# Kernel tuning notes

Hardware: AMD Instinct MI355X
Metric: run time of the kernel (lower is better)

Reference implementation:

```python
import jax, jax.numpy as jnp
import numpy as np

B, C, H, W = 16, 256, 32, 32
N_E, E_DIM = 8192, 256
BETA = 0.25
ENT_RATIO = 0.1
TEMP = 0.01


def _normalize(x, eps=1e-6):
    # torch F.normalize: x / clamp_min(||x||, eps)
    n = jnp.linalg.norm(x, axis=-1, keepdims=True)
    return x / jnp.maximum(n, eps)


def setup_inputs() -> dict:
    key = jax.random.key(0)
    k1, k2, k3 = jax.random.split(key, 3)
    z = jax.random.normal(k1, (B, C, H, W), dtype=jnp.float32)
    # nn.Embedding init: normal(0, e_dim**-0.5)
    emb_weight = jax.random.normal(k2, (N_E, E_DIM), dtype=jnp.float32) * (E_DIM ** -0.5)
    # nn.Linear(e_dim, e_dim)
    proj_w = jax.random.normal(k3, (E_DIM, E_DIM), dtype=jnp.float32) * (E_DIM ** -0.5)
    proj_b = jnp.zeros((E_DIM,), dtype=jnp.float32)
    return {"z": z, "emb_weight": emb_weight, "proj_w": proj_w, "proj_b": proj_b}


def reference(z, emb_weight, proj_w, proj_b):
    sg = jax.lax.stop_gradient
    # SimVQ: project the (frozen) codebook through a linear layer
    weight = emb_weight @ proj_w.T + proj_b            # [K, d]
    b, c, h, w = z.shape
    z_bhwc = jnp.transpose(z, (0, 2, 3, 1))            # [B,H,W,C]
    z_flat = z_bhwc.reshape(b, h * w, c)               # [B,L,C]

    # l2_norm=True branch
    zn = _normalize(z_flat)                             # [B,L,d]
    wn = _normalize(weight)                             # [K,d]

    z2 = jnp.sum(zn * zn, axis=-1, keepdims=True)       # [B,L,1]
    w2 = jnp.sum(wn * wn, axis=-1)[None, None, :]       # [1,1,K]
    dot = jnp.einsum('bld,kd->blk', zn, wn)             # [B,L,K]
    dists = z2 + w2 - 2.0 * dot                         # [B,L,K]

    indices = jnp.argmin(dists, axis=-1)                # [B,L]
    q = wn[indices].reshape(b, h, w, c)                 # gather normalized codebook

    # training losses (l2_norm=True -> compare normalized)
    z_cmp = _normalize(z_bhwc)
    q_cmp = _normalize(q)
    codebook_loss = jnp.mean((q_cmp - sg(z_cmp)) ** 2)
    commit_loss = BETA * jnp.mean((sg(q_cmp) - z_cmp) ** 2)

    # entropy loss on affinity = -dists
    a = (-dists).reshape(-1, dists.shape[-1]) / TEMP    # [B*L, K]
    probs = jax.nn.softmax(a, axis=-1)
    log_probs = jax.nn.log_softmax(a + 1e-5, axis=-1)
    avg_probs = jnp.mean(probs, axis=0)
    avg_entropy = -jnp.sum(avg_probs * jnp.log(avg_probs + 1e-5))
    sample_entropy = -jnp.mean(jnp.sum(probs * log_probs, axis=-1))
    entropy_loss = ENT_RATIO * (sample_entropy - avg_entropy)

    # straight-through estimator, back to channel-first
    z_q = z_bhwc + sg(q - z_bhwc)
    z_q = jnp.transpose(z_q, (0, 3, 1, 2))              # [B,C,H,W]
    flat_indices = indices.reshape(-1)
    return (z_q, codebook_loss, commit_loss, entropy_loss, flat_indices)
```

## Files before the change

### kernel.cpp

```cpp
#include <hip/hip_runtime.h>
#include <math.h>

#define NROWS 16384
#define NCODES 8192
#define DIMS 256
#define NCS 4
#define CEXP 288.5390082f

#define OFF_WN   0u
#define OFF_W2   2097152u
#define OFF_ZN   2105344u
#define OFF_WNH  6299648u
#define OFF_WNL  7348224u
#define OFF_ZNH  8396800u
#define OFF_ZNL  10493952u
#define OFF_PL1  12591104u
#define OFF_PL2  12656640u
#define OFF_PS   12722176u
#define OFF_PI1  12787712u
#define OFF_PI2  12853248u
#define OFF_RM   12918784u
#define OFF_RS   12935168u
#define OFF_RIDX 12951552u
#define OFF_AVGP 12967936u
#define OFF_SCAL 12976128u

typedef __attribute__((ext_vector_type(8))) short bf16x8;
typedef __attribute__((ext_vector_type(4))) float f32x4;
typedef unsigned short u16;

__device__ __forceinline__ u16 f2bf(float f) {
  unsigned u = __float_as_uint(f);
  u += 0x7fffu + ((u >> 16) & 1u);
  return (u16)(u >> 16);
}
__device__ __forceinline__ float bf2f(u16 s) { return __uint_as_float(((unsigned)s) << 16); }

__device__ __forceinline__ void gl_lds16(const u16* g, u16* l) {
  __builtin_amdgcn_global_load_lds(
      (const __attribute__((address_space(1))) unsigned*)g,
      (__attribute__((address_space(3))) unsigned*)l, 16, 0, 0);
}

#define PHASE_BARRIER_CNT()  asm volatile("s_waitcnt vmcnt(4) lgkmcnt(0)\n\ts_barrier" ::: "memory")
#define PHASE_BARRIER_ALL()  asm volatile("s_waitcnt vmcnt(0) lgkmcnt(0)\n\ts_barrier" ::: "memory")
#define DRAIN_VM()           asm volatile("s_waitcnt vmcnt(0)" ::: "memory")

__device__ __forceinline__ void ins2(float x, int idx, float& b1, int& i1, float& b2, int& i2) {
  if (x > b1 || (x == b1 && idx < i1)) { b2 = b1; i2 = i1; b1 = x; i1 = idx; }
  else if (x > b2 || (x == b2 && idx < i2)) { b2 = x; i2 = idx; }
}

__global__ __launch_bounds__(256) void k0_init(float* ws) {
  int i = blockIdx.x * 256 + threadIdx.x;
  if (i < NCODES) ws[OFF_AVGP + i] = 0.f;
  if (i < 16) ws[OFF_SCAL + i] = 0.f;
}

__global__ __launch_bounds__(256) void k1_codebook(const float* __restrict__ emb,
    const float* __restrict__ pw, const float* __restrict__ pb,
    float* __restrict__ wn, float* __restrict__ w2,
    u16* __restrict__ wnh, u16* __restrict__ wnl) {
  __shared__ float e[256];
  __shared__ float red[256];
  int k = blockIdx.x, t = threadIdx.x;
  e[t] = emb[(size_t)k * 256 + t];
  __syncthreads();
  const float4* prow = reinterpret_cast<const float4*>(pw + (size_t)t * 256);
  float acc = pb[t];
  #pragma unroll 8
  for (int q = 0; q < 64; ++q) {
    float4 p4 = prow[q];
    acc += e[q*4+0]*p4.x + e[q*4+1]*p4.y + e[q*4+2]*p4.z + e[q*4+3]*p4.w;
  }
  red[t] = acc * acc;
  __syncthreads();
  for (int s = 128; s; s >>= 1) { if (t < s) red[t] += red[t+s]; __syncthreads(); }
  float inv = 1.f / fmaxf(sqrtf(red[0]), 1e-6f);
  float v = acc * inv;
  size_t o = (size_t)k*256 + t;
  wn[o] = v;
  u16 hb = f2bf(v); float hf = bf2f(hb);
  wnh[o] = hb; wnl[o] = f2bf(v - hf);
  __syncthreads();
  red[t] = v * v;
  __syncthreads();
  for (int s = 128; s; s >>= 1) { if (t < s) red[t] += red[t+s]; __syncthreads(); }
  if (t == 0) w2[k] = red[0];
}

__global__ __launch_bounds__(256) void k2_zn(const float* __restrict__ z,
    float* __restrict__ zn, u16* __restrict__ znh, u16* __restrict__ znl) {
  __shared__ float tile[256][33];
  __shared__ float inv[32];
  int bh = blockIdx.x, t = threadIdx.x;
  const float* zb = z + (size_t)(bh >> 5) * (256*1024) + (size_t)(bh & 31) * 32;
  for (int j = 0; j < 32; ++j) {
    int i = t + j*256; int c = i >> 5, w = i & 31;
    tile[c][w] = zb[(size_t)c*1024 + w];
  }
  __syncthreads();
  if (t < 32) {
    float s = 0.f;
    for (int c = 0; c < 256; ++c) { float v = tile[c][t]; s += v*v; }
    inv[t] = 1.f / fmaxf(sqrtf(s), 1e-6f);
  }
  __syncthreads();
  size_t base = (size_t)bh * 32 * 256;
  for (int w = 0; w < 32; ++w) {
    float v = tile[t][w] * inv[w];
    size_t o = base + (size_t)w*256 + t;
    zn[o] = v;
    u16 hb = f2bf(v); float hf = bf2f(hb);
    znh[o] = hb; znl[o] = f2bf(v - hf);
  }
}

__global__ __attribute__((amdgpu_flat_work_group_size(512,512)))
__attribute__((amdgpu_waves_per_eu(2,2))) void k3_pass1(
    const u16* __restrict__ znh, const u16* __restrict__ znl,
    const u16* __restrict__ wnh, const u16* __restrict__ wnl,
    float* __restrict__ pL1, float* __restrict__ pL2, float* __restrict__ pS,
    int* __restrict__ pI1, int* __restrict__ pI2) {
  __shared__ u16 Cbuf[6][2][128*32];
  int t = threadIdx.x;
  int rb = blockIdx.x >> 2, cs = blockIdx.x & 3;
  int r0 = rb * 256;
  int w = t >> 6, l = t & 63;
  int g = l >> 4, lr = l & 15;
  int slotA = ((lr >> 1) & 3);

  bf16x8 bh[2][8], bl[2][8];
  #pragma unroll
  for (int jr = 0; jr < 2; ++jr) {
    size_t rbase = (size_t)(r0 + w*32 + jr*16 + lr) * 256;
    #pragma unroll
    for (int dc = 0; dc < 8; ++dc) {
      bh[jr][dc] = *(const bf16x8*)&znh[rbase + dc*32 + g*8];
      bl[jr][dc] = *(const bf16x8*)&znl[rbase + dc*32 + g*8];
    }
  }
  #pragma unroll
  for (int jr = 0; jr < 2; ++jr)
    #pragma unroll
    for (int dc = 0; dc < 8; ++dc)
      asm volatile("" : "+v"(bh[jr][dc]), "+v"(bl[jr][dc]));

  const size_t csbase = (size_t)cs * 2048 * 256;
  auto stage = [&](int s, int b) {
    int dc2 = s & 7;
    int krow = (s >> 3) * 128;
    int c = w*16 + (l >> 2);
    int qs = (l & 3) ^ ((l >> 3) & 3);
    size_t go = csbase + (size_t)(krow + c)*256 + dc2*32 + qs*8;
    gl_lds16(&wnh[go], &Cbuf[b][0][w*512]);
    gl_lds16(&wnl[go], &Cbuf[b][1][w*512]);
  };
  DRAIN_VM();
  stage(0, 0);
  stage(1, 1);
  stage(2, 2);
  stage(3, 3);

  float b1[2] = {-3.0e38f, -3.0e38f}, b2[2] = {-3.0e38f, -3.0e38f}, Sv[2] = {0.f, 0.f};
  int i1[2] = {0, 0}, i2[2] = {0, 0};

  for (int kt = 0; kt < 16; ++kt) {
    f32x4 acc[8][2];
    #pragma unroll
    for (int i = 0; i < 8; ++i) { acc[i][0] = (f32x4){0.f,0.f,0.f,0.f}; acc[i][1] = (f32x4){0.f,0.f,0.f,0.f}; }
    #pragma unroll
    for (int dcp = 0; dcp < 4; ++dcp) {
      int s0 = kt*8 + dcp*2;
      if (s0 < 126) PHASE_BARRIER_CNT(); else PHASE_BARRIER_ALL();
      if (s0 + 4 < 128) { int b4 = (s0+4) % 6; stage(s0 + 4, b4); }
      if (s0 + 5 < 128) { int b5 = (s0+5) % 6; stage(s0 + 5, b5); }
      #pragma unroll
      for (int h = 0; h < 2; ++h) {
        int dc = dcp*2 + h;
        int bR = (s0 + h) % 6;
        #pragma unroll
        for (int i = 0; i < 8; ++i) {
          int co = (i*16 + lr)*32 + (g ^ slotA)*8;
          bf16x8 ah = *(const bf16x8*)&Cbuf[bR][0][co];
          bf16x8 al = *(const bf16x8*)&Cbuf[bR][1][co];
          acc[i][0] = __builtin_amdgcn_mfma_f32_16x16x32_bf16(ah, bh[0][dc], acc[i][0], 0, 0, 0);
          acc[i][1] = __builtin_amdgcn_mfma_f32_16x16x32_bf16(ah, bh[1][dc], acc[i][1], 0, 0, 0);
          acc[i][0] = __builtin_amdgcn_mfma_f32_16x16x32_bf16(ah, bl[0][dc], acc[i][0], 0, 0, 0);
          acc[i][1] = __builtin_amdgcn_mfma_f32_16x16x32_bf16(ah, bl[1][dc], acc[i][1], 0, 0, 0);
          acc[i][0] = __builtin_amdgcn_mfma_f32_16x16x32_bf16(al, bh[0][dc], acc[i][0], 0, 0, 0);
          acc[i][1] = __builtin_amdgcn_mfma_f32_16x16x32_bf16(al, bh[1][dc], acc[i][1], 0, 0, 0);
        }
      }
    }
    int kb32 = kt * 32;
    #pragma unroll
    for (int jr = 0; jr < 2; ++jr) {
      float ob1 = b1[jr];
      #pragma unroll
      for (int n = 0; n < 32; ++n) {
        float x = acc[n>>2][jr][n&3];
        bool c1 = x > b1[jr];
        bool c2 = x > b2[jr];
        float hi = fmaxf(x, b1[jr]);
        float lo = fminf(x, b1[jr]);
        b2[jr] = fmaxf(lo, fminf(hi, b2[jr]));
        i2[jr] = c1 ? i1[jr] : (c2 ? (kb32 + n) : i2[jr]);
        b1[jr] = hi;
        i1[jr] = c1 ? (kb32 + n) : i1[jr];
      }
      float negCm = -CEXP * b1[jr];
      float ts0 = 0.f, ts1 = 0.f;
      #pragma unroll
      for (int n = 0; n < 32; n += 2) {
        ts0 += exp2f(fmaf(CEXP, acc[n>>2][jr][n&3],     negCm));
        ts1 += exp2f(fmaf(CEXP, acc[(n+1)>>2][jr][(n+1)&3], negCm));
      }
      Sv[jr] = Sv[jr] * exp2f(CEXP * (ob1 - b1[jr])) + (ts0 + ts1);
    }
  }
  float my[2], y2[2]; int gi1[2], gi2[2];
  #pragma unroll
  for (int jr = 0; jr < 2; ++jr) {
    int e1 = i1[jr], e2 = i2[jr];
    int base = cs*2048 + g*4;
    gi1[jr] = base + (e1>>5)*128 + ((e1>>2)&7)*16 + (e1&3);
    gi2[jr] = base + (e2>>5)*128 + ((e2>>2)&7)*16 + (e2&3);
    my[jr] = CEXP * b1[jr];
    y2[jr] = CEXP * b2[jr];
    #pragma unroll
    for (int mask = 16; mask <= 32; mask <<= 1) {
      float om  = __shfl_xor(my[jr], mask, 64);
      float oy2 = __shfl_xor(y2[jr], mask, 64);
      float oS  = __shfl_xor(Sv[jr], mask, 64);
      int   o1  = __shfl_xor(gi1[jr], mask, 64);
      int   o2  = __shfl_xor(gi2[jr], mask, 64);
      float pm = my[jr];
      ins2(om,  o1, my[jr], gi1[jr], y2[jr], gi2[jr]);
      ins2(oy2, o2, my[jr], gi1[jr], y2[jr], gi2[jr]);
      Sv[jr] = Sv[jr] * exp2f(pm - my[jr]) + oS * exp2f(om - my[jr]);
    }
  }
  if (g == 0) {
    #pragma unroll
    for (int jr = 0; jr < 2; ++jr) {
      int r = r0 + w*32 + jr*16 + lr;
      size_t o = (size_t)cs * NROWS + r;
      pL1[o] = my[jr]; pL2[o] = y2[jr]; pS[o] = Sv[jr];
      pI1[o] = gi1[jr]; pI2[o] = gi2[jr];
    }
  }
}

__global__ __launch_bounds__(256) void k3b_refine(
    const float* __restrict__ zn, const float* __restrict__ wn, const float* __restrict__ w2,
    const float* __restrict__ pL1, const float* __restrict__ pL2, const float* __restrict__ pS,
    const int* __restrict__ pI1, const int* __restrict__ pI2,
    float* __restrict__ rm, float* __restrict__ rs, int* __restrict__ ridx) {
  int t = threadIdx.x;
  int r = blockIdx.x * 4 + (t >> 6);
  int l = t & 63;
  float b1 = pL1[r], b2 = pL2[r], S = pS[r];
  int i1 = pI1[r], i2 = pI2[r];
  #pragma unroll
  for (int c = 1; c < NCS; ++c) {
    size_t o = (size_t)c * NROWS + r;
    float ob1 = pL1[o], ob2 = pL2[o], oS = pS[o];
    int oi1 = pI1[o], oi2 = pI2[o];
    float pb1 = b1;
    ins2(ob1, oi1, b1, i1, b2, i2);
    ins2(ob2, oi2, b1, i1, b2, i2);
    S = S * exp2f(pb1 - b1) + oS * exp2f(ob1 - b1);
  }
  int cand = (l < 32) ? i1 : i2;
  int lo = l & 31;
  const float* zr = zn + (size_t)r * 256;
  const float* wc = wn + (size_t)cand * 256;
  float d = 0.f;
  #pragma unroll
  for (int q = 0; q < 8; ++q) d += zr[lo + q*32] * wc[lo + q*32];
  #pragma unroll
  for (int mask = 1; mask <= 16; mask <<= 1) d += __shfl_xor(d, mask, 64);
  float dOther = __shfl_xor(d, 32, 64);
  if (l == 0) {
    float s1 = w2[i1] - 2.f*d;
    float s2 = w2[i2] - 2.f*dOther;
    int win = i1;
    if (s2 < s1 || (s2 == s1 && i2 < i1)) win = i2;
    rm[r] = b1; rs[r] = S; ridx[r] = win;
  }
}

__global__ __attribute__((amdgpu_flat_work_group_size(512,512)))
__attribute__((amdgpu_waves_per_eu(2,2))) void k4_pass2(
    const u16* __restrict__ znh, const u16* __restrict__ znl,
    const u16* __restrict__ wnh, const u16* __restrict__ wnl,
    const float* __restrict__ rm, const float* __restrict__ rs,
    float* __restrict__ avgp, float* __restrict__ scal) {
  __shared__ u16 Cbuf[6][2][128*32];
  __shared__ float avgSlice[2048];
  __shared__ float red[512];
  int t = threadIdx.x;
  int rb = blockIdx.x >> 2, cs = blockIdx.x & 3;
  int r0 = rb * 256;
  int w = t >> 6, l = t & 63;
  int g = l >> 4, lr = l & 15;
  int slotA = ((lr >> 1) & 3);

  for (int i = t; i < 2048; i += 512) avgSlice[i] = 0.f;

  bf16x8 bh[2][8], bl[2][8];
  #pragma unroll
  for (int jr = 0; jr < 2; ++jr) {
    size_t rbase = (size_t)(r0 + w*32 + jr*16 + lr) * 256;
    #pragma unroll
    for (int dc = 0; dc < 8; ++dc) {
      bh[jr][dc] = *(const bf16x8*)&znh[rbase + dc*32 + g*8];
      bl[jr][dc] = *(const bf16x8*)&znl[rbase + dc*32 + g*8];
    }
  }
  #pragma unroll
  for (int jr = 0; jr < 2; ++jr)
    #pragma unroll
    for (int dc = 0; dc < 8; ++dc)
      asm volatile("" : "+v"(bh[jr][dc]), "+v"(bl[jr][dc]));

  float m_[2], invS[2], l2s[2];
  #pragma unroll
  for (int jr = 0; jr < 2; ++jr) {
    int r = r0 + w*32 + jr*16 + lr;
    float mm = rm[r], ss = rs[r];
    m_[jr] = mm; invS[jr] = 1.f / ss; l2s[jr] = log2f(ss);
  }

  const size_t csbase = (size_t)cs * 2048 * 256;
  auto stage = [&](int s, int b) {
    int dc2 = s & 7;
    int krow = (s >> 3) * 128;
    int c = w*16 + (l >> 2);
    int qs = (l & 3) ^ ((l >> 3) & 3);
    size_t go = csbase + (size_t)(krow + c)*256 + dc2*32 + qs*8;
    gl_lds16(&wnh[go], &Cbuf[b][0][w*512]);
    gl_lds16(&wnl[go], &Cbuf[b][1][w*512]);
  };
  DRAIN_VM();
  stage(0, 0);
  stage(1, 1);
  stage(2, 2);
  stage(3, 3);
  float ent = 0.f;

  for (int kt = 0; kt < 16; ++kt) {
    f32x4 acc[8][2];
    #pragma unroll
    for (int i = 0; i < 8; ++i) { acc[i][0] = (f32x4){0.f,0.f,0.f,0.f}; acc[i][1] = (f32x4){0.f,0.f,0.f,0.f}; }
    #pragma unroll
    for (int dcp = 0; dcp < 4; ++dcp) {
      int s0 = kt*8 + dcp*2;
      if (s0 < 126) PHASE_BARRIER_CNT(); else PHASE_BARRIER_ALL();
      if (s0 + 4 < 128) { int b4 = (s0+4) % 6; stage(s0 + 4, b4); }
      if (s0 + 5 < 128) { int b5 = (s0+5) % 6; stage(s0 + 5, b5); }
      #pragma unroll
      for (int h = 0; h < 2; ++h) {
        int dc = dcp*2 + h;
        int bR = (s0 + h) % 6;
        #pragma unroll
        for (int i = 0; i < 8; ++i) {
          int co = (i*16 + lr)*32 + (g ^ slotA)*8;
          bf16x8 ah = *(const bf16x8*)&Cbuf[bR][0][co];
          bf16x8 al = *(const bf16x8*)&Cbuf[bR][1][co];
          acc[i][0] = __builtin_amdgcn_mfma_f32_16x16x32_bf16(ah, bh[0][dc], acc[i][0], 0, 0, 0);
          acc[i][1] = __builtin_amdgcn_mfma_f32_16x16x32_bf16(ah, bh[1][dc], acc[i][1], 0, 0, 0);
          acc[i][0] = __builtin_amdgcn_mfma_f32_16x16x32_bf16(ah, bl[0][dc], acc[i][0], 0, 0, 0);
          acc[i][1] = __builtin_amdgcn_mfma_f32_16x16x32_bf16(ah, bl[1][dc], acc[i][1], 0, 0, 0);
          acc[i][0] = __builtin_amdgcn_mfma_f32_16x16x32_bf16(al, bh[0][dc], acc[i][0], 0, 0, 0);
          acc[i][1] = __builtin_amdgcn_mfma_f32_16x16x32_bf16(al, bh[1][dc], acc[i][1], 0, 0, 0);
        }
      }
    }
    #pragma unroll
    for (int half = 0; half < 2; ++half) {
      float ca[16];
      #pragma unroll
      for (int n = 0; n < 16; ++n) ca[n] = 0.f;
      #pragma unroll
      for (int jr = 0; jr < 2; ++jr) {
        float is = invS[jr], l2 = l2s[jr];
        #pragma unroll
        for (int ii = 0; ii < 4; ++ii) {
          int i = half*4 + ii;
          #pragma unroll
          for (int v = 0; v < 4; ++v) {
            float tt = fmaf(CEXP, acc[i][jr][v], -m_[jr]);
            float p = exp2f(tt) * is;
            ent -= p * (tt - l2);
            ca[ii*4+v] += p;
          }
        }
      }
      #pragma unroll
      for (int n = 0; n < 16; ++n) {
        float sv = ca[n];
        sv += __shfl_xor(sv, 1, 64);
        sv += __shfl_xor(sv, 2, 64);
        sv += __shfl_xor(sv, 4, 64);
        sv += __shfl_xor(sv, 8, 64);
        if (lr == 0)
          atomicAdd(&avgSlice[kt*128 + (half*4 + (n>>2))*16 + g*4 + (n&3)], sv);
      }
    }
  }
  __syncthreads();
  for (int i = t; i < 2048; i += 512)
    atomicAdd(&avgp[cs*2048 + i], avgSlice[i] * (1.f/16384.f));
  red[t] = ent;
  __syncthreads();
  for (int s2 = 256; s2; s2 >>= 1) { if (t < s2) red[t] += red[t + s2]; __syncthreads(); }
  if (t == 0) atomicAdd(&scal[1], red[0] * 0.6931471806f);
}

__global__ __launch_bounds__(256) void k5_gather(const float* __restrict__ zn,
    const float* __restrict__ wn, const int* __restrict__ row_idx,
    float* __restrict__ out_zq, float* __restrict__ scal) {
  __shared__ float tile[256][33];
  __shared__ float red4[4];
  __shared__ float red[256];
  int bh = blockIdx.x, t = threadIdx.x;
  int b = bh >> 5, h = bh & 31;
  float cb = 0.f;
  for (int w = 0; w < 32; ++w) {
    int r = bh*32 + w;
    int idx = row_idx[r];
    float q = wn[(size_t)idx*256 + t];
    float s = q*q;
    #pragma unroll
    for (int mask = 32; mask; mask >>= 1) s += __shfl_xor(s, mask, 64);
    if ((t & 63) == 0) red4[t >> 6] = s;
    __syncthreads();
    float tot = red4[0] + red4[1] + red4[2] + red4[3];
    float inv = 1.f / fmaxf(sqrtf(tot), 1e-6f);
    float zv = zn[(size_t)r*256 + t];
    float d = q*inv - zv;
    cb += d*d;
    tile[t][w] = q;
    __syncthreads();
  }
  red[t] = cb;
  __syncthreads();
  for (int s2 = 128; s2; s2 >>= 1) { if (t < s2) red[t] += red[t+s2]; __syncthreads(); }
  if (t == 0) atomicAdd(&scal[0], red[0]);
  float* ob = out_zq + (size_t)b*256*1024 + (size_t)h*32;
  for (int j = 0; j < 32; ++j) {
    int i = t + j*256; int c = i >> 5, ww = i & 31;
    ob[(size_t)c*1024 + ww] = tile[c][ww];
  }
}

__global__ __launch_bounds__(256) void k6_final(const float* __restrict__ avg_probs,
    const float* __restrict__ scal, const int* __restrict__ row_idx,
    float* __restrict__ out) {
  int t = threadIdx.x;
  if (blockIdx.x < 64) {
    int r = blockIdx.x*256 + t;
    out[4194307 + r] = (float)row_idx[r];
    return;
  }
  __shared__ float red[256];
  float s = 0.f;
  for (int j = 0; j < 32; ++j) {
    float v = avg_probs[t + j*256];
    s -= v * logf(v + 1e-5f);
  }
  red[t] = s;
  __syncthreads();
  for (int q = 128; q; q >>= 1) { if (t < q) red[t] += red[t+q]; __syncthreads(); }
  if (t == 0) {
    float avg_entropy = red[0];
    float sample_entropy = scal[1] * (1.f/16384.f);
    float cb = scal[0] * (1.f/4194304.f);
    out[4194304] = cb;
    out[4194305] = 0.25f * cb;
    out[4194306] = 0.1f * (sample_entropy - avg_entropy);
  }
}

extern "C" void kernel_launch(void* const* d_in, const int* in_sizes, int n_in,
                              void* d_out, int out_size, void* d_ws, size_t ws_size,
                              hipStream_t stream) {
  const float* z   = (const float*)d_in[0];
  const float* emb = (const float*)d_in[1];
  const float* pw  = (const float*)d_in[2];
  const float* pb  = (const float*)d_in[3];
  float* ws  = (float*)d_ws;
  float* out = (float*)d_out;
  float* wn   = ws + OFF_WN;
  float* w2   = ws + OFF_W2;
  float* zn   = ws + OFF_ZN;
  u16*   wnh  = (u16*)(ws + OFF_WNH);
  u16*   wnl  = (u16*)(ws + OFF_WNL);
  u16*   znh  = (u16*)(ws + OFF_ZNH);
  u16*   znl  = (u16*)(ws + OFF_ZNL);
  float* pL1  = ws + OFF_PL1;
  float* pL2  = ws + OFF_PL2;
  float* pS   = ws + OFF_PS;
  int*   pI1  = (int*)(ws + OFF_PI1);
  int*   pI2  = (int*)(ws + OFF_PI2);
  float* rm   = ws + OFF_RM;
  float* rs   = ws + OFF_RS;
  int*   ridx = (int*)(ws + OFF_RIDX);
  float* avgp = ws + OFF_AVGP;
  float* scal = ws + OFF_SCAL;

  k0_init<<<32, 256, 0, stream>>>(ws);
  k1_codebook<<<NCODES, 256, 0, stream>>>(emb, pw, pb, wn, w2, wnh, wnl);
  k2_zn<<<512, 256, 0, stream>>>(z, zn, znh, znl);
  k3_pass1<<<256, 512, 0, stream>>>(znh, znl, wnh, wnl, pL1, pL2, pS, pI1, pI2);
  k3b_refine<<<NROWS/4, 256, 0, stream>>>(zn, wn, w2, pL1, pL2, pS, pI1, pI2, rm, rs, ridx);
  k4_pass2<<<256, 512, 0, stream>>>(znh, znl, wnh, wnl, rm, rs, avgp, scal);
  k5_gather<<<512, 256, 0, stream>>>(zn, wn, ridx, out, scal);
  k6_final<<<65, 256, 0, stream>>>(avgp, scal, ridx, out);
}
```

Measured before the change: 782.1 us.

## Halve rows per block in both GEMM passes and double the grid size

```diff
diff --git a/kernel.cpp b/kernel.cpp
--- a/kernel.cpp
+++ b/kernel.cpp
@@ -125,26 +125,20 @@
   __shared__ u16 Cbuf[6][2][128*32];
   int t = threadIdx.x;
   int rb = blockIdx.x >> 2, cs = blockIdx.x & 3;
-  int r0 = rb * 256;
+  int r0 = rb * 128;
   int w = t >> 6, l = t & 63;
   int g = l >> 4, lr = l & 15;
   int slotA = ((lr >> 1) & 3);
 
-  bf16x8 bh[2][8], bl[2][8];
-  #pragma unroll
-  for (int jr = 0; jr < 2; ++jr) {
-    size_t rbase = (size_t)(r0 + w*32 + jr*16 + lr) * 256;
+  bf16x8 bh[8], bl[8];
+  {
+    size_t rbase = (size_t)(r0 + w*16 + lr) * 256;
     #pragma unroll
     for (int dc = 0; dc < 8; ++dc) {
-      bh[jr][dc] = *(const bf16x8*)&znh[rbase + dc*32 + g*8];
-      bl[jr][dc] = *(const bf16x8*)&znl[rbase + dc*32 + g*8];
-    }
-  }
-  #pragma unroll
-  for (int jr = 0; jr < 2; ++jr)
-    #pragma unroll
-    for (int dc = 0; dc < 8; ++dc)
-      asm volatile("" : "+v"(bh[jr][dc]), "+v"(bl[jr][dc]));
+      bh[dc] = *(const bf16x8*)&znh[rbase + dc*32 + g*8];
+      bl[dc] = *(const bf16x8*)&znl[rbase + dc*32 + g*8];
+    }
+  }
 
   const size_t csbase = (size_t)cs * 2048 * 256;
   auto stage = [&](int s, int b) {
@@ -162,13 +156,13 @@
   stage(2, 2);
   stage(3, 3);
 
-  float b1[2] = {-3.0e38f, -3.0e38f}, b2[2] = {-3.0e38f, -3.0e38f}, Sv[2] = {0.f, 0.f};
-  int i1[2] = {0, 0}, i2[2] = {0, 0};
+  float b1 = -3.0e38f, b2 = -3.0e38f, Sv = 0.f;
+  int i1 = 0, i2 = 0;
 
   for (int kt = 0; kt < 16; ++kt) {
-    f32x4 acc[8][2];
-    #pragma unroll
-    for (int i = 0; i < 8; ++i) { acc[i][0] = (f32x4){0.f,0.f,0.f,0.f}; acc[i][1] = (f32x4){0.f,0.f,0.f,0.f}; }
+    f32x4 acc[8];
+    #pragma unroll
+    for (int i = 0; i < 8; ++i) acc[i] = (f32x4){0.f,0.f,0.f,0.f};
     #pragma unroll
     for (int dcp = 0; dcp < 4; ++dcp) {
       int s0 = kt*8 + dcp*2;
@@ -184,71 +178,62 @@
           int co = (i*16 + lr)*32 + (g ^ slotA)*8;
           bf16x8 ah = *(const bf16x8*)&Cbuf[bR][0][co];
           bf16x8 al = *(const bf16x8*)&Cbuf[bR][1][co];
-          acc[i][0] = __builtin_amdgcn_mfma_f32_16x16x32_bf16(ah, bh[0][dc], acc[i][0], 0, 0, 0);
-          acc[i][1] = __builtin_amdgcn_mfma_f32_16x16x32_bf16(ah, bh[1][dc], acc[i][1], 0, 0, 0);
-          acc[i][0] = __builtin_amdgcn_mfma_f32_16x16x32_bf16(ah, bl[0][dc], acc[i][0], 0, 0, 0);
-          acc[i][1] = __builtin_amdgcn_mfma_f32_16x16x32_bf16(ah, bl[1][dc], acc[i][1], 0, 0, 0);
-          acc[i][0] = __builtin_amdgcn_mfma_f32_16x16x32_bf16(al, bh[0][dc], acc[i][0], 0, 0, 0);
-          acc[i][1] = __builtin_amdgcn_mfma_f32_16x16x32_bf16(al, bh[1][dc], acc[i][1], 0, 0, 0);
+          acc[i] = __builtin_amdgcn_mfma_f32_16x16x32_bf16(ah, bh[dc], acc[i], 0, 0, 0);
+          acc[i] = __builtin_amdgcn_mfma_f32_16x16x32_bf16(ah, bl[dc], acc[i], 0, 0, 0);
+          acc[i] = __builtin_amdgcn_mfma_f32_16x16x32_bf16(al, bh[dc], acc[i], 0, 0, 0);
         }
       }
     }
     int kb32 = kt * 32;
-    #pragma unroll
-    for (int jr = 0; jr < 2; ++jr) {
-      float ob1 = b1[jr];
+    {
+      float ob1 = b1;
       #pragma unroll
       for (int n = 0; n < 32; ++n) {
-        float x = acc[n>>2][jr][n&3];
-        bool c1 = x > b1[jr];
-        bool c2 = x > b2[jr];
-        float hi = fmaxf(x, b1[jr]);
-        float lo = fminf(x, b1[jr]);
-        b2[jr] = fmaxf(lo, fminf(hi, b2[jr]));
-        i2[jr] = c1 ? i1[jr] : (c2 ? (kb32 + n) : i2[jr]);
-        b1[jr] = hi;
-        i1[jr] = c1 ? (kb32 + n) : i1[jr];
-      }
-      float negCm = -CEXP * b1[jr];
+        float x = acc[n>>2][n&3];
+        bool c1 = x > b1;
+        bool c2 = x > b2;
+        float hi = fmaxf(x, b1);
+        float lo = fminf(x, b1);
+        b2 = fmaxf(lo, fminf(hi, b2));
+        i2 = c1 ? i1 : (c2 ? (kb32 + n) : i2);
+        b1 = hi;
+        i1 = c1 ? (kb32 + n) : i1;
+      }
+      float negCm = -CEXP * b1;
       float ts0 = 0.f, ts1 = 0.f;
       #pragma unroll
       for (int n = 0; n < 32; n += 2) {
-        ts0 += exp2f(fmaf(CEXP, acc[n>>2][jr][n&3],     negCm));
-        ts1 += exp2f(fmaf(CEXP, acc[(n+1)>>2][jr][(n+1)&3], negCm));
-      }
-      Sv[jr] = Sv[jr] * exp2f(CEXP * (ob1 - b1[jr])) + (ts0 + ts1);
-    }
-  }
-  float my[2], y2[2]; int gi1[2], gi2[2];
-  #pragma unroll
-  for (int jr = 0; jr < 2; ++jr) {
-    int e1 = i1[jr], e2 = i2[jr];
+        ts0 += exp2f(fmaf(CEXP, acc[n>>2][n&3],         negCm));
+        ts1 += exp2f(fmaf(CEXP, acc[(n+1)>>2][(n+1)&3], negCm));
+      }
+      Sv = Sv * exp2f(CEXP * (ob1 - b1)) + (ts0 + ts1);
+    }
+  }
+  float my, y2; int gi1, gi2;
+  {
     int base = cs*2048 + g*4;
-    gi1[jr] = base + (e1>>5)*128 + ((e1>>2)&7)*16 + (e1&3);
-    gi2[jr] = base + (e2>>5)*128 + ((e2>>2)&7)*16 + (e2&3);
-    my[jr] = CEXP * b1[jr];
-    y2[jr] = CEXP * b2[jr];
+    gi1 = base + (i1>>5)*128 + ((i1>>2)&7)*16 + (i1&3);
+    gi2 = base + (i2>>5)*128 + ((i2>>2)&7)*16 + (i2&3);
+    my = CEXP * b1;
+    y2 = CEXP * b2;
     #pragma unroll
     for (int mask = 16; mask <= 32; mask <<= 1) {
-      float om  = __shfl_xor(my[jr], mask, 64);
-      float oy2 = __shfl_xor(y2[jr], mask, 64);
-      float oS  = __shfl_xor(Sv[jr], mask, 64);
-      int   o1  = __shfl_xor(gi1[jr], mask, 64);
-      int   o2  = __shfl_xor(gi2[jr], mask, 64);
-      float pm = my[jr];
-      ins2(om,  o1, my[jr], gi1[jr], y2[jr], gi2[jr]);
-      ins2(oy2, o2, my[jr], gi1[jr], y2[jr], gi2[jr]);
-      Sv[jr] = Sv[jr] * exp2f(pm - my[jr]) + oS * exp2f(om - my[jr]);
+      float om  = __shfl_xor(my, mask, 64);
+      float oy2 = __shfl_xor(y2, mask, 64);
+      float oS  = __shfl_xor(Sv, mask, 64);
+      int   o1  = __shfl_xor(gi1, mask, 64);
+      int   o2  = __shfl_xor(gi2, mask, 64);
+      float pm = my;
+      ins2(om,  o1, my, gi1, y2, gi2);
+      ins2(oy2, o2, my, gi1, y2, gi2);
+      Sv = Sv * exp2f(pm - my) + oS * exp2f(om - my);
     }
   }
   if (g == 0) {
-    #pragma unroll
-    for (int jr = 0; jr < 2; ++jr) {
-      int r = r0 + w*32 + jr*16 + lr;
-      size_t o = (size_t)cs * NROWS + r;
-      pL1[o] = my[jr]; pL2[o] = y2[jr]; pS[o] = Sv[jr];
-      pI1[o] = gi1[jr]; pI2[o] = gi2[jr];
-    }
+    int r = r0 + w*16 + lr;
+    size_t o = (size_t)cs * NROWS + r;
+    pL1[o] = my; pL2[o] = y2; pS[o] = Sv;
+    pI1[o] = gi1; pI2[o] = gi2;
   }
 }
 
@@ -302,35 +287,27 @@
   __shared__ float red[512];
   int t = threadIdx.x;
   int rb = blockIdx.x >> 2, cs = blockIdx.x & 3;
-  int r0 = rb * 256;
+  int r0 = rb * 128;
   int w = t >> 6, l = t & 63;
   int g = l >> 4, lr = l & 15;
   int slotA = ((lr >> 1) & 3);
 
   for (int i = t; i < 2048; i += 512) avgSlice[i] = 0.f;
 
-  bf16x8 bh[2][8], bl[2][8];
-  #pragma unroll
-  for (int jr = 0; jr < 2; ++jr) {
-    size_t rbase = (size_t)(r0 + w*32 + jr*16 + lr) * 256;
+  bf16x8 bh[8], bl[8];
+  {
+    size_t rbase = (size_t)(r0 + w*16 + lr) * 256;
     #pragma unroll
     for (int dc = 0; dc < 8; ++dc) {
-      bh[jr][dc] = *(const bf16x8*)&znh[rbase + dc*32 + g*8];
-      bl[jr][dc] = *(const bf16x8*)&znl[rbase + dc*32 + g*8];
-    }
-  }
-  #pragma unroll
-  for (int jr = 0; jr < 2; ++jr)
-    #pragma unroll
-    for (int dc = 0; dc < 8; ++dc)
-      asm volatile("" : "+v"(bh[jr][dc]), "+v"(bl[jr][dc]));
-
-  float m_[2], invS[2], l2s[2];
-  #pragma unroll
-  for (int jr = 0; jr < 2; ++jr) {
-    int r = r0 + w*32 + jr*16 + lr;
+      bh[dc] = *(const bf16x8*)&znh[rbase + dc*32 + g*8];
+      bl[dc] = *(const bf16x8*)&znl[rbase + dc*32 + g*8];
+    }
+  }
+  float m_, invS, l2s;
+  {
+    int r = r0 + w*16 + lr;
     float mm = rm[r], ss = rs[r];
-    m_[jr] = mm; invS[jr] = 1.f / ss; l2s[jr] = log2f(ss);
+    m_ = mm; invS = 1.f / ss; l2s = log2f(ss);
   }
 
   const size_t csbase = (size_t)cs * 2048 * 256;
@@ -351,9 +328,9 @@
   float ent = 0.f;
 
   for (int kt = 0; kt < 16; ++kt) {
-    f32x4 acc[8][2];
-    #pragma unroll
-    for (int i = 0; i < 8; ++i) { acc[i][0] = (f32x4){0.f,0.f,0.f,0.f}; acc[i][1] = (f32x4){0.f,0.f,0.f,0.f}; }
+    f32x4 acc[8];
+    #pragma unroll
+    for (int i = 0; i < 8; ++i) acc[i] = (f32x4){0.f,0.f,0.f,0.f};
     #pragma unroll
     for (int dcp = 0; dcp < 4; ++dcp) {
       int s0 = kt*8 + dcp*2;
@@ -369,33 +346,27 @@
           int co = (i*16 + lr)*32 + (g ^ slotA)*8;
           bf16x8 ah = *(const bf16x8*)&Cbuf[bR][0][co];
           bf16x8 al = *(const bf16x8*)&Cbuf[bR][1][co];
-          acc[i][0] = __builtin_amdgcn_mfma_f32_16x16x32_bf16(ah, bh[0][dc], acc[i][0], 0, 0, 0);
-          acc[i][1] = __builtin_amdgcn_mfma_f32_16x16x32_bf16(ah, bh[1][dc], acc[i][1], 0, 0, 0);
-          acc[i][0] = __builtin_amdgcn_mfma_f32_16x16x32_bf16(ah, bl[0][dc], acc[i][0], 0, 0, 0);
-          acc[i][1] = __builtin_amdgcn_mfma_f32_16x16x32_bf16(ah, bl[1][dc], acc[i][1], 0, 0, 0);
-          acc[i][0] = __builtin_amdgcn_mfma_f32_16x16x32_bf16(al, bh[0][dc], acc[i][0], 0, 0, 0);
-          acc[i][1] = __builtin_amdgcn_mfma_f32_16x16x32_bf16(al, bh[1][dc], acc[i][1], 0, 0, 0);
+          acc[i] = __builtin_amdgcn_mfma_f32_16x16x32_bf16(ah, bh[dc], acc[i], 0, 0, 0);
+          acc[i] = __builtin_amdgcn_mfma_f32_16x16x32_bf16(ah, bl[dc], acc[i], 0, 0, 0);
+          acc[i] = __builtin_amdgcn_mfma_f32_16x16x32_bf16(al, bh[dc], acc[i], 0, 0, 0);
         }
       }
     }
+    int kb = cs*2048 + kt*128;
     #pragma unroll
     for (int half = 0; half < 2; ++half) {
       float ca[16];
       #pragma unroll
       for (int n = 0; n < 16; ++n) ca[n] = 0.f;
       #pragma unroll
-      for (int jr = 0; jr < 2; ++jr) {
-        float is = invS[jr], l2 = l2s[jr];
+      for (int ii = 0; ii < 4; ++ii) {
+        int i = half*4 + ii;
         #pragma unroll
-        for (int ii = 0; ii < 4; ++ii) {
-          int i = half*4 + ii;
-          #pragma unroll
-          for (int v = 0; v < 4; ++v) {
-            float tt = fmaf(CEXP, acc[i][jr][v], -m_[jr]);
-            float p = exp2f(tt) * is;
-            ent -= p * (tt - l2);
-            ca[ii*4+v] += p;
-          }
+        for (int v = 0; v < 4; ++v) {
+          float tt = fmaf(CEXP, acc[i][v], -m_);
+          float p = exp2f(tt) * invS;
+          ent -= p * (tt - l2s);
+          ca[ii*4+v] += p;
         }
       }
       #pragma unroll
@@ -514,9 +485,9 @@
   k0_init<<<32, 256, 0, stream>>>(ws);
   k1_codebook<<<NCODES, 256, 0, stream>>>(emb, pw, pb, wn, w2, wnh, wnl);
   k2_zn<<<512, 256, 0, stream>>>(z, zn, znh, znl);
-  k3_pass1<<<256, 512, 0, stream>>>(znh, znl, wnh, wnl, pL1, pL2, pS, pI1, pI2);
+  k3_pass1<<<512, 512, 0, stream>>>(znh, znl, wnh, wnl, pL1, pL2, pS, pI1, pI2);
   k3b_refine<<<NROWS/4, 256, 0, stream>>>(zn, wn, w2, pL1, pL2, pS, pI1, pI2, rm, rs, ridx);
-  k4_pass2<<<256, 512, 0, stream>>>(znh, znl, wnh, wnl, rm, rs, avgp, scal);
+  k4_pass2<<<512, 512, 0, stream>>>(znh, znl, wnh, wnl, rm, rs, avgp, scal);
   k5_gather<<<512, 256, 0, stream>>>(zn, wn, ridx, out, scal);
   k6_final<<<65, 256, 0, stream>>>(avgp, scal, ridx, out);
 }
```

After: 889.6 us. +13.7%, slower.
